# Kernel tuning notes

Hardware: AMD Instinct MI355X
Metric: run time of the kernel (lower is better)

The kernel has to match this reference:

```python
import jax, jax.numpy as jnp
import numpy as np

B, T = 64, 40  # hardcoded in original forward via pos.view(64, 40, 2)


def _gat(x, src, dst, W, a_src, a_dst, b):
    # PyG GATConv (concat=True): linear, per-edge attention, softmax over dst neighborhoods, scatter-sum
    H, C = a_src.shape
    n = x.shape[0]
    h = (x @ W).reshape(n, H, C)
    logits = jax.nn.leaky_relu((h * a_src).sum(-1)[src] + (h * a_dst).sum(-1)[dst], 0.2)  # [E,H]
    logits = logits - jax.ops.segment_max(logits, dst, num_segments=n)[dst]
    e = jnp.exp(logits)
    alpha = e / (jax.ops.segment_sum(e, dst, num_segments=n)[dst] + 1e-16)  # [E,H]
    out = jax.ops.segment_sum(h[src] * alpha[:, :, None], dst, num_segments=n)  # [N,H,C]
    return out.reshape(n, H * C) + b


def _bn(x, g, b):
    # training-mode BatchNorm over the node dimension (biased variance, eps=1e-5)
    mu = x.mean(0)
    var = x.var(0)
    return g * (x - mu) / jnp.sqrt(var + 1e-5) + b


def setup_inputs() -> dict:
    key = jax.random.key(0)
    ks = jax.random.split(key, 20)
    N, E, Fin, H, C1, C2 = 2560, 327680, 62, 4, 64, 64
    sc = 0.05
    x = jax.random.normal(ks[0], (N, Fin), jnp.float32)
    src = jax.random.randint(ks[1], (E,), 0, N)
    dst = (src + jax.random.randint(ks[2], (E,), 1, N)) % N  # no self-loops by construction
    edge_index = jnp.stack([src, dst])
    pos = jax.random.normal(ks[3], (N, 2), jnp.float32)
    mask = jnp.ones((N,), jnp.float32)
    batch = jnp.zeros((N,), jnp.int32)
    return {
        "x": x, "edge_index": edge_index, "pos": pos, "mask": mask, "batch": batch,
        "W1": jax.random.normal(ks[4], (Fin + 2, H * C1), jnp.float32) * sc,
        "a_src1": jax.random.normal(ks[5], (H, C1), jnp.float32) * sc,
        "a_dst1": jax.random.normal(ks[6], (H, C1), jnp.float32) * sc,
        "b1": jnp.zeros((H * C1,), jnp.float32),
        "g1": jnp.ones((H * C1,), jnp.float32),
        "be1": jnp.zeros((H * C1,), jnp.float32),
        "W2": jax.random.normal(ks[7], (H * C1, H * C2), jnp.float32) * sc,
        "a_src2": jax.random.normal(ks[8], (H, C2), jnp.float32) * sc,
        "a_dst2": jax.random.normal(ks[9], (H, C2), jnp.float32) * sc,
        "b2": jnp.zeros((H * C2,), jnp.float32),
        "g2": jnp.ones((H * C2,), jnp.float32),
        "be2": jnp.zeros((H * C2,), jnp.float32),
        "Wf": jax.random.normal(ks[10], (H * C2, 2), jnp.float32) * sc,
        "bf": jnp.zeros((2,), jnp.float32),
    }


def reference(x, edge_index, pos, mask, batch, W1, a_src1, a_dst1, b1, g1, be1,
              W2, a_src2, a_dst2, b2, g2, be2, Wf, bf):
    n = x.shape[0]
    src, dst = edge_index[0], edge_index[1]
    # recompute_features: per-edge distance/angle, scatter_add onto source node
    d = pos[dst] - pos[src]  # [E,2]
    ef = jnp.stack([jnp.sqrt((d * d).sum(-1)), jnp.arctan2(d[:, 1], d[:, 0])], axis=1)
    agg = jax.ops.segment_sum(ef, src, num_segments=n)  # [N,2]
    xf = jnp.concatenate([x, agg], axis=1)
    # GATConv adds self-loops by default
    loops = jnp.arange(n)
    s = jnp.concatenate([src, loops])
    t = jnp.concatenate([dst, loops])
    h = jax.nn.relu(_bn(_gat(xf, s, t, W1, a_src1, a_dst1, b1), g1, be1))
    h = jax.nn.relu(_bn(_gat(h, s, t, W2, a_src2, a_dst2, b2), g2, be2))
    out = (h @ Wf + bf) * mask[:, None]
    out_node = out.reshape(B, T, 2)
    updated_pos = pos.reshape(B, T, 2) + out_node
    return out_node, updated_pos
```

## Files before the change

### kernel.cpp

```cpp
#include <hip/hip_runtime.h>
#include <hip/hip_fp16.h>
#include <math.h>

typedef unsigned short u16;

#define NN 2560
#define EE 327680
#define HC 256
#define FIN 62
#define CAP 240
#define NCH 16
#define CHSZ (EE / NCH)
#define PCAP 64

__device__ __forceinline__ float lrelu(float x) { return x >= 0.f ? x : 0.2f * x; }
__device__ __forceinline__ float ldh(const __half* p, int i) { return __half2float(p[i]); }

__global__ void k_init(int* __restrict__ cntd, int* __restrict__ cnts,
                       u16* __restrict__ esrcB) {
  int n = blockIdx.x * 256 + threadIdx.x;
  if (n >= NN) return;
  cntd[n] = 1;
  cnts[n] = 0;
  esrcB[n * CAP] = (u16)n;
}

__global__ void k_bin(const int* __restrict__ src, const int* __restrict__ dst,
                      int* __restrict__ cntd, int* __restrict__ cnts,
                      u16* __restrict__ esrcB, u16* __restrict__ edstB) {
  __shared__ u16 bufD[64][PCAP];
  __shared__ u16 bufS[64][PCAP];
  __shared__ int cD[64], cS[64], baseD[64], baseS[64];
  int t = threadIdx.x;
  int c = blockIdx.x;
  int r = blockIdx.y;
  if (t < 64) { cD[t] = 0; cS[t] = 0; }
  __syncthreads();
  int e0 = c * CHSZ;
  for (int i = t; i < CHSZ; i += 256) {
    int e = e0 + i;
    int s = src[e], d = dst[e];
    if ((d >> 6) == r) {
      int p = atomicAdd(&cD[d & 63], 1);
      if (p < PCAP) bufD[d & 63][p] = (u16)s;
    }
    if ((s >> 6) == r) {
      int q = atomicAdd(&cS[s & 63], 1);
      if (q < PCAP) bufS[s & 63][q] = (u16)d;
    }
  }
  __syncthreads();
  if (t < 64) baseD[t] = atomicAdd(&cntd[r * 64 + t], min(cD[t], PCAP));
  else if (t < 128) baseS[t - 64] = atomicAdd(&cnts[r * 64 + (t - 64)], min(cS[t - 64], PCAP));
  __syncthreads();
  for (int idx = t; idx < 64 * PCAP; idx += 256) {
    int n = idx >> 6;
    int i = idx & 63;
    if (i < min(cD[n], PCAP)) esrcB[(r * 64 + n) * CAP + baseD[n] + i] = bufD[n][i];
    if (i < min(cS[n], PCAP)) edstB[(r * 64 + n) * CAP + baseS[n] + i] = bufS[n][i];
  }
}

__global__ void k_edge_gather(const int* __restrict__ cnts, const u16* __restrict__ edstB,
                              const float* __restrict__ pos, float* __restrict__ agg) {
  int n = blockIdx.x, l = threadIdx.x;
  int cnt = min(cnts[n], CAP);
  float2 ps = ((const float2*)pos)[n];
  float dsum = 0.f, asum = 0.f;
  for (int i = l; i < cnt; i += 64) {
    int d = (int)edstB[n * CAP + i];
    float2 pd = ((const float2*)pos)[d];
    float dx = pd.x - ps.x, dy = pd.y - ps.y;
    dsum += sqrtf(dx * dx + dy * dy);
    asum += atan2f(dy, dx);
  }
  for (int o = 32; o > 0; o >>= 1) {
    dsum += __shfl_down(dsum, o);
    asum += __shfl_down(asum, o);
  }
  if (l == 0) { agg[2 * n] = dsum; agg[2 * n + 1] = asum; }
}

__global__ void k_gemm1(const float* __restrict__ x, const float* __restrict__ agg,
                        const float* __restrict__ W, const float* __restrict__ a_src,
                        const float* __restrict__ a_dst,
                        __half* __restrict__ Hout, float* __restrict__ asb,
                        float* __restrict__ adb) {
  __shared__ float xrow[4][64];
  int n0 = blockIdx.x * 4, t = threadIdx.x;
  int m0 = t >> 6, i0 = t & 63;
  xrow[m0][i0] = (i0 < FIN) ? x[(n0 + m0) * FIN + i0] : agg[(n0 + m0) * 2 + (i0 - FIN)];
  __syncthreads();
  float a0 = 0.f, a1 = 0.f, a2 = 0.f, a3 = 0.f;
#pragma unroll 8
  for (int k = 0; k < 64; ++k) {
    float w = W[k * HC + t];
    a0 += xrow[0][k] * w; a1 += xrow[1][k] * w;
    a2 += xrow[2][k] * w; a3 += xrow[3][k] * w;
  }
  Hout[(n0 + 0) * HC + t] = __float2half(a0);
  Hout[(n0 + 1) * HC + t] = __float2half(a1);
  Hout[(n0 + 2) * HC + t] = __float2half(a2);
  Hout[(n0 + 3) * HC + t] = __float2half(a3);
  float accs[4] = {a0, a1, a2, a3};
  int h = t >> 6, lane = t & 63;
  float vs = a_src[t], vdd = a_dst[t];
#pragma unroll
  for (int m = 0; m < 4; ++m) {
    float p1 = accs[m] * vs;
    float p2 = accs[m] * vdd;
    for (int o = 32; o > 0; o >>= 1) {
      p1 += __shfl_down(p1, o);
      p2 += __shfl_down(p2, o);
    }
    if (lane == 0) {
      asb[(n0 + m) * 4 + h] = p1;
      adb[(n0 + m) * 4 + h] = p2;
    }
  }
}

__global__ void k_gemm2(const __half* __restrict__ X, const float* __restrict__ mu,
                        const float* __restrict__ rinv, const float* __restrict__ g,
                        const float* __restrict__ be, const float* __restrict__ W,
                        const float* __restrict__ a_src, const float* __restrict__ a_dst,
                        __half* __restrict__ Hout, float* __restrict__ asb,
                        float* __restrict__ adb) {
  __shared__ float xrow[4][256];
  int n0 = blockIdx.x * 4, t = threadIdx.x;
  float bmu = mu[t], brv = rinv[t], bg = g[t], bb = be[t];
#pragma unroll
  for (int m = 0; m < 4; ++m)
    xrow[m][t] = fmaxf((ldh(X, (n0 + m) * HC + t) - bmu) * brv * bg + bb, 0.f);
  __syncthreads();
  float a0 = 0.f, a1 = 0.f, a2 = 0.f, a3 = 0.f;
#pragma unroll 4
  for (int k = 0; k < 256; ++k) {
    float w = W[k * HC + t];
    a0 += xrow[0][k] * w; a1 += xrow[1][k] * w;
    a2 += xrow[2][k] * w; a3 += xrow[3][k] * w;
  }
  Hout[(n0 + 0) * HC + t] = __float2half(a0);
  Hout[(n0 + 1) * HC + t] = __float2half(a1);
  Hout[(n0 + 2) * HC + t] = __float2half(a2);
  Hout[(n0 + 3) * HC + t] = __float2half(a3);
  float accs[4] = {a0, a1, a2, a3};
  int h = t >> 6, lane = t & 63;
  float vs = a_src[t], vdd = a_dst[t];
#pragma unroll
  for (int m = 0; m < 4; ++m) {
    float p1 = accs[m] * vs;
    float p2 = accs[m] * vdd;
    for (int o = 32; o > 0; o >>= 1) {
      p1 += __shfl_down(p1, o);
      p2 += __shfl_down(p2, o);
    }
    if (lane == 0) {
      asb[(n0 + m) * 4 + h] = p1;
      adb[(n0 + m) * 4 + h] = p2;
    }
  }
}

__global__ void k_agg(const int* __restrict__ cntd, const u16* __restrict__ esrcB,
                      const float* __restrict__ asb, const float* __restrict__ adb,
                      const __half* __restrict__ Hin, const float* __restrict__ bias,
                      __half* __restrict__ Out) {
  __shared__ float eE[4][256];
  __shared__ int sS[256];
  __shared__ float wred[4][4];
  int n = blockIdx.x, t = threadIdx.x;
  int h = t >> 6, lane = t & 63;
  int cnt = min(cntd[n], CAP);

  float ad0 = adb[n * 4 + 0], ad1 = adb[n * 4 + 1];
  float ad2 = adb[n * 4 + 2], ad3 = adb[n * 4 + 3];

  float e0 = 0.f, e1 = 0.f, e2 = 0.f, e3 = 0.f;
  int s = 0;
  if (t < cnt) {
    s = (int)esrcB[n * CAP + t];
    e0 = expf(lrelu(asb[s * 4 + 0] + ad0));
    e1 = expf(lrelu(asb[s * 4 + 1] + ad1));
    e2 = expf(lrelu(asb[s * 4 + 2] + ad2));
    e3 = expf(lrelu(asb[s * 4 + 3] + ad3));
  }
  eE[0][t] = e0; eE[1][t] = e1; eE[2][t] = e2; eE[3][t] = e3;
  sS[t] = s;
  __syncthreads();

  float acc = 0.f;
#pragma unroll 4
  for (int j = 0; j < cnt; ++j) {
    acc += eE[h][j] * ldh(Hin, sS[j] * HC + t);
  }

  float d0 = e0, d1 = e1, d2 = e2, d3 = e3;
  for (int o = 32; o > 0; o >>= 1) {
    d0 += __shfl_down(d0, o);
    d1 += __shfl_down(d1, o);
    d2 += __shfl_down(d2, o);
    d3 += __shfl_down(d3, o);
  }
  if (lane == 0) {
    wred[h][0] = d0; wred[h][1] = d1; wred[h][2] = d2; wred[h][3] = d3;
  }
  __syncthreads();
  float denom = wred[0][h] + wred[1][h] + wred[2][h] + wred[3][h];
  Out[n * HC + t] = __float2half(acc / (denom + 1e-16f) + bias[t]);
}

__global__ void k_bnstats(const __half* __restrict__ X, float* __restrict__ mu,
                          float* __restrict__ rinv) {
  __shared__ float rs[256];
  __shared__ float rq[256];
  int f = blockIdx.x, t = threadIdx.x;
  float s = 0.f, sq = 0.f;
  for (int n = t; n < NN; n += 256) {
    float v = ldh(X, n * HC + f);
    s += v;
    sq += v * v;
  }
  rs[t] = s; rq[t] = sq;
  __syncthreads();
  for (int o = 128; o > 0; o >>= 1) {
    if (t < o) { rs[t] += rs[t + o]; rq[t] += rq[t + o]; }
    __syncthreads();
  }
  if (t == 0) {
    float m = rs[0] / NN;
    float var = rq[0] / NN - m * m;
    mu[f] = m;
    rinv[f] = rsqrtf(var + 1e-5f);
  }
}

__global__ void k_final(const __half* __restrict__ X, const float* __restrict__ mu,
                        const float* __restrict__ rinv, const float* __restrict__ g,
                        const float* __restrict__ be, const float* __restrict__ Wf,
                        const float* __restrict__ bfv, const float* __restrict__ mask,
                        const float* __restrict__ pos, float* __restrict__ out) {
  int n = blockIdx.x, l = threadIdx.x;
  float r0 = 0.f, r1 = 0.f;
  for (int c = l; c < HC; c += 64) {
    float v = fmaxf((ldh(X, n * HC + c) - mu[c]) * rinv[c] * g[c] + be[c], 0.f);
    r0 += v * Wf[c * 2];
    r1 += v * Wf[c * 2 + 1];
  }
  for (int o = 32; o > 0; o >>= 1) {
    r0 += __shfl_down(r0, o);
    r1 += __shfl_down(r1, o);
  }
  if (l == 0) {
    float mk = mask[n];
    float o0 = (r0 + bfv[0]) * mk;
    float o1 = (r1 + bfv[1]) * mk;
    out[n * 2]     = o0;
    out[n * 2 + 1] = o1;
    out[2 * NN + n * 2]     = pos[n * 2]     + o0;
    out[2 * NN + n * 2 + 1] = pos[n * 2 + 1] + o1;
  }
}

extern "C" void kernel_launch(void* const* d_in, const int* in_sizes, int n_in,
                              void* d_out, int out_size, void* d_ws, size_t ws_size,
                              hipStream_t stream) {
  (void)in_sizes; (void)n_in; (void)out_size; (void)ws_size;
  const float* x    = (const float*)d_in[0];
  const int*   ei   = (const int*)d_in[1];
  const float* pos  = (const float*)d_in[2];
  const float* mask = (const float*)d_in[3];
  const float* W1   = (const float*)d_in[5];
  const float* as1  = (const float*)d_in[6];
  const float* ad1  = (const float*)d_in[7];
  const float* b1   = (const float*)d_in[8];
  const float* g1   = (const float*)d_in[9];
  const float* be1  = (const float*)d_in[10];
  const float* W2   = (const float*)d_in[11];
  const float* as2  = (const float*)d_in[12];
  const float* ad2  = (const float*)d_in[13];
  const float* b2   = (const float*)d_in[14];
  const float* g2   = (const float*)d_in[15];
  const float* be2  = (const float*)d_in[16];
  const float* Wf   = (const float*)d_in[17];
  const float* bfv  = (const float*)d_in[18];

  const int* srcp = ei;
  const int* dstp = ei + EE;

  float* ws   = (float*)d_ws;
  float* agg  = ws;
  float* asb  = agg + 5120;
  float* adb  = asb + 10240;
  float* mu   = adb + 10240;
  float* rinv = mu + 256;
  int* cntd   = (int*)(rinv + 256);
  int* cnts   = cntd + 2560;
  u16* esrcB  = (u16*)(cnts + 2560);
  __half* o   = (__half*)(esrcB + 2560 * CAP);
  __half* h   = o + 655360;
  u16* edstB  = (u16*)h;

  k_init<<<(NN + 255) / 256, 256, 0, stream>>>(cntd, cnts, esrcB);
  dim3 grid_bin(NCH, NN / 64);
  k_bin<<<grid_bin, 256, 0, stream>>>(srcp, dstp, cntd, cnts, esrcB, edstB);
  k_edge_gather<<<NN, 64, 0, stream>>>(cnts, edstB, pos, agg);

  k_gemm1<<<NN / 4, 256, 0, stream>>>(x, agg, W1, as1, ad1, h, asb, adb);
  k_agg<<<NN, 256, 0, stream>>>(cntd, esrcB, asb, adb, h, b1, o);
  k_bnstats<<<HC, 256, 0, stream>>>(o, mu, rinv);

  k_gemm2<<<NN / 4, 256, 0, stream>>>(o, mu, rinv, g1, be1, W2, as2, ad2, h, asb, adb);
  k_agg<<<NN, 256, 0, stream>>>(cntd, esrcB, asb, adb, h, b2, o);
  k_bnstats<<<HC, 256, 0, stream>>>(o, mu, rinv);

  k_final<<<NN, 64, 0, stream>>>(o, mu, rinv, g2, be2, Wf, bfv, mask, pos, (float*)d_out);
}
```

Before: 125.9 us.

## Fuse edge-feature aggregation into binning kernel and vectorize edge loads

Removes the separate source-side edge bucket and the k_edge_gather kernel, and computes each edge's distance and angle directly in k_bin. These are accumulated through shared-memory float atomics and then global atomics into agg, which k_init now zeroes. Edge indices are loaded as int4. The chunk count doubles while the per-block buffer capacity halves, with an overflow path that writes straight to global memory through a global atomic. This trades one kernel launch and the edstB round trip for extra atomics and transcendental work inside the binning grid. Float atomic accumulation also makes the summation order nondeterministic.

```diff
diff --git a/kernel.cpp b/kernel.cpp
--- a/kernel.cpp
+++ b/kernel.cpp
@@ -9,76 +9,75 @@
 #define HC 256
 #define FIN 62
 #define CAP 240
-#define NCH 16
+#define NCH 32
 #define CHSZ (EE / NCH)
-#define PCAP 64
+#define PCAP 32
 
 __device__ __forceinline__ float lrelu(float x) { return x >= 0.f ? x : 0.2f * x; }
 __device__ __forceinline__ float ldh(const __half* p, int i) { return __half2float(p[i]); }
 
-__global__ void k_init(int* __restrict__ cntd, int* __restrict__ cnts,
-                       u16* __restrict__ esrcB) {
+__global__ void k_init(int* __restrict__ cntd, u16* __restrict__ esrcB,
+                       float* __restrict__ agg) {
   int n = blockIdx.x * 256 + threadIdx.x;
   if (n >= NN) return;
   cntd[n] = 1;
-  cnts[n] = 0;
   esrcB[n * CAP] = (u16)n;
+  agg[2 * n] = 0.f;
+  agg[2 * n + 1] = 0.f;
 }
 
 __global__ void k_bin(const int* __restrict__ src, const int* __restrict__ dst,
-                      int* __restrict__ cntd, int* __restrict__ cnts,
-                      u16* __restrict__ esrcB, u16* __restrict__ edstB) {
+                      const float* __restrict__ pos, int* __restrict__ cntd,
+                      u16* __restrict__ esrcB, float* __restrict__ agg) {
   __shared__ u16 bufD[64][PCAP];
-  __shared__ u16 bufS[64][PCAP];
-  __shared__ int cD[64], cS[64], baseD[64], baseS[64];
+  __shared__ int cD[64], baseD[64];
+  __shared__ float aggD[64], aggA[64];
   int t = threadIdx.x;
   int c = blockIdx.x;
   int r = blockIdx.y;
-  if (t < 64) { cD[t] = 0; cS[t] = 0; }
+  if (t < 64) { cD[t] = 0; aggD[t] = 0.f; aggA[t] = 0.f; }
   __syncthreads();
   int e0 = c * CHSZ;
-  for (int i = t; i < CHSZ; i += 256) {
-    int e = e0 + i;
-    int s = src[e], d = dst[e];
-    if ((d >> 6) == r) {
-      int p = atomicAdd(&cD[d & 63], 1);
-      if (p < PCAP) bufD[d & 63][p] = (u16)s;
-    }
-    if ((s >> 6) == r) {
-      int q = atomicAdd(&cS[s & 63], 1);
-      if (q < PCAP) bufS[s & 63][q] = (u16)d;
+  const int4* s4p = (const int4*)(src + e0);
+  const int4* d4p = (const int4*)(dst + e0);
+  for (int i = t; i < CHSZ / 4; i += 256) {
+    int4 s4 = s4p[i];
+    int4 d4 = d4p[i];
+    int ss[4] = {s4.x, s4.y, s4.z, s4.w};
+    int dd[4] = {d4.x, d4.y, d4.z, d4.w};
+#pragma unroll
+    for (int k = 0; k < 4; ++k) {
+      int s = ss[k], d = dd[k];
+      if ((d >> 6) == r) {
+        int p = atomicAdd(&cD[d & 63], 1);
+        if (p < PCAP) {
+          bufD[d & 63][p] = (u16)s;
+        } else {
+          int idx = atomicAdd(&cntd[d], 1);
+          esrcB[d * CAP + idx] = (u16)s;
+        }
+      }
+      if ((s >> 6) == r) {
+        float2 psv = ((const float2*)pos)[s];
+        float2 pdv = ((const float2*)pos)[d];
+        float dx = pdv.x - psv.x, dy = pdv.y - psv.y;
+        atomicAdd(&aggD[s & 63], sqrtf(dx * dx + dy * dy));
+        atomicAdd(&aggA[s & 63], atan2f(dy, dx));
+      }
     }
   }
   __syncthreads();
   if (t < 64) baseD[t] = atomicAdd(&cntd[r * 64 + t], min(cD[t], PCAP));
-  else if (t < 128) baseS[t - 64] = atomicAdd(&cnts[r * 64 + (t - 64)], min(cS[t - 64], PCAP));
   __syncthreads();
   for (int idx = t; idx < 64 * PCAP; idx += 256) {
-    int n = idx >> 6;
-    int i = idx & 63;
+    int n = idx >> 5;
+    int i = idx & 31;
     if (i < min(cD[n], PCAP)) esrcB[(r * 64 + n) * CAP + baseD[n] + i] = bufD[n][i];
-    if (i < min(cS[n], PCAP)) edstB[(r * 64 + n) * CAP + baseS[n] + i] = bufS[n][i];
-  }
-}
-
-__global__ void k_edge_gather(const int* __restrict__ cnts, const u16* __restrict__ edstB,
-                              const float* __restrict__ pos, float* __restrict__ agg) {
-  int n = blockIdx.x, l = threadIdx.x;
-  int cnt = min(cnts[n], CAP);
-  float2 ps = ((const float2*)pos)[n];
-  float dsum = 0.f, asum = 0.f;
-  for (int i = l; i < cnt; i += 64) {
-    int d = (int)edstB[n * CAP + i];
-    float2 pd = ((const float2*)pos)[d];
-    float dx = pd.x - ps.x, dy = pd.y - ps.y;
-    dsum += sqrtf(dx * dx + dy * dy);
-    asum += atan2f(dy, dx);
-  }
-  for (int o = 32; o > 0; o >>= 1) {
-    dsum += __shfl_down(dsum, o);
-    asum += __shfl_down(asum, o);
-  }
-  if (l == 0) { agg[2 * n] = dsum; agg[2 * n + 1] = asum; }
+  }
+  if (t < 64) {
+    atomicAdd(&agg[2 * (r * 64 + t)], aggD[t]);
+    atomicAdd(&agg[2 * (r * 64 + t) + 1], aggA[t]);
+  }
 }
 
 __global__ void k_gemm1(const float* __restrict__ x, const float* __restrict__ agg,
@@ -295,16 +294,13 @@
   float* mu   = adb + 10240;
   float* rinv = mu + 256;
   int* cntd   = (int*)(rinv + 256);
-  int* cnts   = cntd + 2560;
-  u16* esrcB  = (u16*)(cnts + 2560);
+  u16* esrcB  = (u16*)(cntd + 2560);
   __half* o   = (__half*)(esrcB + 2560 * CAP);
   __half* h   = o + 655360;
-  u16* edstB  = (u16*)h;
-
-  k_init<<<(NN + 255) / 256, 256, 0, stream>>>(cntd, cnts, esrcB);
+
+  k_init<<<(NN + 255) / 256, 256, 0, stream>>>(cntd, esrcB, agg);
   dim3 grid_bin(NCH, NN / 64);
-  k_bin<<<grid_bin, 256, 0, stream>>>(srcp, dstp, cntd, cnts, esrcB, edstB);
-  k_edge_gather<<<NN, 64, 0, stream>>>(cnts, edstB, pos, agg);
+  k_bin<<<grid_bin, 256, 0, stream>>>(srcp, dstp, pos, cntd, esrcB, agg);
 
   k_gemm1<<<NN / 4, 256, 0, stream>>>(x, agg, W1, as1, ad1, h, asb, adb);
   k_agg<<<NN, 256, 0, stream>>>(cntd, esrcB, asb, adb, h, b1, o);
```

After: 122.0 us, median of 2. 3.1% less time.
